# Performance work log

Measured on AMD Instinct MI355X. Metric: run time of the kernel, lower is better.

Reference implementation:

```python
import jax, jax.numpy as jnp
import numpy as np
import math

D_MODEL = 512
H = 8
D_K = D_MODEL // H


def setup_inputs() -> dict:
    key = jax.random.key(0)
    ks = jax.random.split(key, 12)
    B, T = 4, 1024
    q = jax.random.normal(ks[0], (B, T, D_MODEL), jnp.float32)
    k = jax.random.normal(ks[1], (B, T, D_MODEL), jnp.float32)
    v = jax.random.normal(ks[2], (B, T, D_MODEL), jnp.float32)
    mask = jnp.ones((B, T), jnp.int32)
    prev = jax.random.normal(ks[3], (B, H, T, T), jnp.float32)
    s = 1.0 / math.sqrt(D_MODEL)
    w_q = jax.random.normal(ks[4], (D_MODEL, D_MODEL), jnp.float32) * s
    w_k = jax.random.normal(ks[5], (D_MODEL, D_MODEL), jnp.float32) * s
    w_v = jax.random.normal(ks[6], (D_MODEL, D_MODEL), jnp.float32) * s
    w_o = jax.random.normal(ks[7], (D_MODEL, D_MODEL), jnp.float32) * s
    # Conv2d weights: torch layout OIHW; init std=0.01 per _init_conv_weights
    tw = jax.random.normal(ks[8], (H, H, 3, 3), jnp.float32) * 0.01
    tb = jnp.zeros((H,), jnp.float32)
    aw = jax.random.normal(ks[9], (H, 2 * H, 3, 3), jnp.float32) * 0.01
    ab = jnp.zeros((H,), jnp.float32)
    return {"q": q, "k": k, "v": v, "mask": mask, "previous_attention_scores": prev,
            "w_q": w_q, "w_k": w_k, "w_v": w_v, "w_o": w_o,
            "tw": tw, "tb": tb, "aw": aw, "ab": ab}


def _conv2d(x, w, b):
    # x: [B,C,T,T], w: [O,I,3,3] (torch OIHW), padding=1
    y = jax.lax.conv_general_dilated(
        x, w, window_strides=(1, 1), padding=((1, 1), (1, 1)),
        dimension_numbers=("NCHW", "OIHW", "NCHW"))
    return y + b[None, :, None, None]


def reference(q, k, v, mask, previous_attention_scores, w_q, w_k, w_v, w_o, tw, tb, aw, ab):
    B, T, _ = q.shape
    # torch Linear: y = x @ W^T  (W is [out,in])
    query = (q @ w_q.T).reshape(B, T, H, D_K).transpose(0, 2, 1, 3)  # [B,H,T,d_k]
    key = (k @ w_k.T).reshape(B, T, H, D_K).transpose(0, 2, 1, 3)
    value = (v @ w_v.T).reshape(B, T, H, D_K).transpose(0, 2, 1, 3)

    M = jnp.einsum("bhqd,bhkd->bhqk", query, key)  # [B,H,T,T]
    Mt = _conv2d(previous_attention_scores, tw, tb)
    Ma = _conv2d(jnp.concatenate((M, Mt), axis=1), aw, ab)

    A = Ma / math.sqrt(D_K)
    m = mask[:, None, None, :]  # [B,1,1,T]
    A = jnp.where(m == 0, -1e9, A)
    A = jax.nn.softmax(A, axis=-1)

    out = jnp.einsum("bhqk,bhkd->bhqd", A, value)
    out = out.transpose(0, 2, 1, 3).reshape(B, T, D_MODEL)
    return out @ w_o.T, A
```

## Files before the change

### kernel.cpp

```cpp
#include <hip/hip_runtime.h>
#include <hip/hip_bf16.h>

#define B_ 4
#define T_ 1024
#define DM 512
#define H_ 8
#define DK 64

typedef __attribute__((ext_vector_type(4))) float f32x4;
typedef __attribute__((ext_vector_type(8))) short bf16x8;

__device__ __forceinline__ unsigned short f2bf(float f) {
  __hip_bfloat16 h = __float2bfloat16(f);
  return *reinterpret_cast<unsigned short*>(&h);
}

__device__ __forceinline__ void split2(float x, short& hi, short& lo) {
  unsigned short h = f2bf(x);
  float fh = __uint_as_float(((unsigned)h) << 16);
  unsigned short l = f2bf(x - fh);
  hi = (short)h; lo = (short)l;
}

template<int OMODE, int OUTBF>
__global__ __launch_bounds__(256)
void proj_mfma(const float* __restrict__ X, const float* __restrict__ W,
               void* __restrict__ outv, int M, int N, int K) {
  float* out = (float*)outv;
  unsigned short* outb = (unsigned short*)outv;
  __shared__ __align__(16) unsigned short Ah[2048], Al[2048];
  __shared__ __align__(16) unsigned short Bh[2048], Bl[2048];
  const int t = threadIdx.x;
  const int n0 = blockIdx.x * 64, m0 = blockIdx.y * 64;
  const int wave = t >> 6, lane = t & 63;
  const int lrow = lane & 15, quad = lane >> 4;
  const int wm = wave & 1, wn = wave >> 1;
  const int srow = t >> 2, skc = t & 3;
  const int sbase = srow * 32 + ((skc ^ ((srow >> 1) & 3)) * 8);
  const int cswz = quad ^ ((lrow >> 1) & 3);
  f32x4 acc[2][2] = {};

  for (int k0 = 0; k0 < K; k0 += 32) {
    {
      const float* p = &X[(long)(m0 + srow) * K + k0 + skc * 8];
      float4 v0 = *(const float4*)p, v1 = *(const float4*)(p + 4);
      float xs[8] = {v0.x, v0.y, v0.z, v0.w, v1.x, v1.y, v1.z, v1.w};
      bf16x8 hh, ll;
#pragma unroll
      for (int i = 0; i < 8; ++i) { short h, l; split2(xs[i], h, l); hh[i] = h; ll[i] = l; }
      *(bf16x8*)&Ah[sbase] = hh; *(bf16x8*)&Al[sbase] = ll;
    }
    {
      const float* p = &W[(long)(n0 + srow) * K + k0 + skc * 8];
      float4 v0 = *(const float4*)p, v1 = *(const float4*)(p + 4);
      float xs[8] = {v0.x, v0.y, v0.z, v0.w, v1.x, v1.y, v1.z, v1.w};
      bf16x8 hh, ll;
#pragma unroll
      for (int i = 0; i < 8; ++i) { short h, l; split2(xs[i], h, l); hh[i] = h; ll[i] = l; }
      *(bf16x8*)&Bh[sbase] = hh; *(bf16x8*)&Bl[sbase] = ll;
    }
    __syncthreads();
    bf16x8 ahv[2], alv[2], bhv[2], blv[2];
#pragma unroll
    for (int f = 0; f < 2; ++f) {
      int ra = (wm * 32 + f * 16 + lrow) * 32 + cswz * 8;
      ahv[f] = *(const bf16x8*)&Ah[ra];
      alv[f] = *(const bf16x8*)&Al[ra];
      int rb = (wn * 32 + f * 16 + lrow) * 32 + cswz * 8;
      bhv[f] = *(const bf16x8*)&Bh[rb];
      blv[f] = *(const bf16x8*)&Bl[rb];
    }
#pragma unroll
    for (int fi = 0; fi < 2; ++fi)
#pragma unroll
      for (int fj = 0; fj < 2; ++fj) {
        acc[fi][fj] = __builtin_amdgcn_mfma_f32_16x16x32_bf16(alv[fi], bhv[fj], acc[fi][fj], 0, 0, 0);
        acc[fi][fj] = __builtin_amdgcn_mfma_f32_16x16x32_bf16(ahv[fi], blv[fj], acc[fi][fj], 0, 0, 0);
        acc[fi][fj] = __builtin_amdgcn_mfma_f32_16x16x32_bf16(ahv[fi], bhv[fj], acc[fi][fj], 0, 0, 0);
      }
    __syncthreads();
  }

#pragma unroll
  for (int fi = 0; fi < 2; ++fi)
#pragma unroll
    for (int fj = 0; fj < 2; ++fj)
#pragma unroll
      for (int r = 0; r < 4; ++r) {
        int row = m0 + wm * 32 + fi * 16 + quad * 4 + r;
        int col = n0 + wn * 32 + fj * 16 + lrow;
        float v = acc[fi][fj][r];
        if (OMODE == 0) {
          out[(long)row * N + col] = v;
        } else {
          int b = row >> 10, tt = row & 1023, h = col >> 6, d = col & 63;
          long off = ((long)(b * H_ + h) * T_ + tt) * DK + d;
          if (OUTBF) outb[off] = f2bf(v);
          else       out[off] = v;
        }
      }
}

__global__ __launch_bounds__(256)
void softmax_av(float* __restrict__ A, const float* __restrict__ Vp,
                float* __restrict__ ctx, const int* __restrict__ mask) {
  __shared__ __align__(16) unsigned short Ah[2048], Al[2048];
  __shared__ __align__(16) unsigned short Bh[2048], Bl[2048];
  __shared__ float sm[64][4], ss[64][4];
  const int t = threadIdx.x;
  const int bh = blockIdx.y, b = bh >> 3, h = bh & 7;
  const int m0 = blockIdx.x * 64;
  A += (long)bh * T_ * T_;
  const float* V = Vp + (long)bh * T_ * DK;
  const int wave = t >> 6, lane = t & 63;
  const int lrow = lane & 15, quad = lane >> 4;
  const int wm = wave & 1, wn = wave >> 1;
  const int srow = t >> 2, skc = t & 3;
  float* arow_p = &A[(long)(m0 + srow) * T_];

  float pm = -3.0e38f, ps = 0.f;
  {
    const int cb = skc * 256;
    for (int c = 0; c < 256; c += 4) {
      float4 v = *(const float4*)&arow_p[cb + c];
      int4 mk = *(const int4*)&mask[b * T_ + cb + c];
      float x0 = mk.x ? v.x : -1e9f;
      float x1 = mk.y ? v.y : -1e9f;
      float x2 = mk.z ? v.z : -1e9f;
      float x3 = mk.w ? v.w : -1e9f;
      float m4 = fmaxf(fmaxf(x0, x1), fmaxf(x2, x3));
      if (m4 > pm) { ps *= __expf(pm - m4); pm = m4; }
      ps += __expf(x0 - pm) + __expf(x1 - pm) + __expf(x2 - pm) + __expf(x3 - pm);
    }
  }
  sm[srow][skc] = pm; ss[srow][skc] = ps;
  __syncthreads();
  const float rmx = fmaxf(fmaxf(sm[srow][0], sm[srow][1]),
                          fmaxf(sm[srow][2], sm[srow][3]));
  const float rsum = ss[srow][0] * __expf(sm[srow][0] - rmx)
                   + ss[srow][1] * __expf(sm[srow][1] - rmx)
                   + ss[srow][2] * __expf(sm[srow][2] - rmx)
                   + ss[srow][3] * __expf(sm[srow][3] - rmx);
  const float rinv = 1.0f / rsum;

  const int sbase = srow * 32 + ((skc ^ ((srow >> 1) & 3)) * 8);
  const int vn = t & 63, vkg = t >> 6;
  const int bbase = vn * 32 + ((vkg ^ ((vn >> 1) & 3)) * 8);
  const int cswz = quad ^ ((lrow >> 1) & 3);
  f32x4 acc[2][2] = {};

  for (int k0 = 0; k0 < T_; k0 += 32) {
    __syncthreads();
    {
      float* p = &arow_p[k0 + skc * 8];
      float4 v0 = *(const float4*)p, v1 = *(const float4*)(p + 4);
      int4 mk0 = *(const int4*)&mask[b * T_ + k0 + skc * 8];
      int4 mk1 = *(const int4*)&mask[b * T_ + k0 + skc * 8 + 4];
      float e[8];
      e[0] = __expf((mk0.x ? v0.x : -1e9f) - rmx) * rinv;
      e[1] = __expf((mk0.y ? v0.y : -1e9f) - rmx) * rinv;
      e[2] = __expf((mk0.z ? v0.z : -1e9f) - rmx) * rinv;
      e[3] = __expf((mk0.w ? v0.w : -1e9f) - rmx) * rinv;
      e[4] = __expf((mk1.x ? v1.x : -1e9f) - rmx) * rinv;
      e[5] = __expf((mk1.y ? v1.y : -1e9f) - rmx) * rinv;
      e[6] = __expf((mk1.z ? v1.z : -1e9f) - rmx) * rinv;
      e[7] = __expf((mk1.w ? v1.w : -1e9f) - rmx) * rinv;
      *(float4*)p = make_float4(e[0], e[1], e[2], e[3]);
      *(float4*)(p + 4) = make_float4(e[4], e[5], e[6], e[7]);
      bf16x8 hh, ll;
#pragma unroll
      for (int i = 0; i < 8; ++i) { short hi_, lo_; split2(e[i], hi_, lo_); hh[i] = hi_; ll[i] = lo_; }
      *(bf16x8*)&Ah[sbase] = hh; *(bf16x8*)&Al[sbase] = ll;
    }
    {
      bf16x8 hh, ll;
#pragma unroll
      for (int j = 0; j < 8; ++j) {
        float x = V[(long)(k0 + vkg * 8 + j) * DK + vn];
        short hi_, lo_; split2(x, hi_, lo_); hh[j] = hi_; ll[j] = lo_;
      }
      *(bf16x8*)&Bh[bbase] = hh; *(bf16x8*)&Bl[bbase] = ll;
    }
    __syncthreads();
    bf16x8 ahv[2], alv[2], bhv[2], blv[2];
#pragma unroll
    for (int f = 0; f < 2; ++f) {
      int ra = (wm * 32 + f * 16 + lrow) * 32 + cswz * 8;
      ahv[f] = *(const bf16x8*)&Ah[ra];
      alv[f] = *(const bf16x8*)&Al[ra];
      int rb = (wn * 32 + f * 16 + lrow) * 32 + cswz * 8;
      bhv[f] = *(const bf16x8*)&Bh[rb];
      blv[f] = *(const bf16x8*)&Bl[rb];
    }
#pragma unroll
    for (int fi = 0; fi < 2; ++fi)
#pragma unroll
      for (int fj = 0; fj < 2; ++fj) {
        acc[fi][fj] = __builtin_amdgcn_mfma_f32_16x16x32_bf16(alv[fi], bhv[fj], acc[fi][fj], 0, 0, 0);
        acc[fi][fj] = __builtin_amdgcn_mfma_f32_16x16x32_bf16(ahv[fi], blv[fj], acc[fi][fj], 0, 0, 0);
        acc[fi][fj] = __builtin_amdgcn_mfma_f32_16x16x32_bf16(ahv[fi], bhv[fj], acc[fi][fj], 0, 0, 0);
      }
  }

#pragma unroll
  for (int fi = 0; fi < 2; ++fi)
#pragma unroll
    for (int fj = 0; fj < 2; ++fj)
#pragma unroll
      for (int r = 0; r < 4; ++r) {
        int row = m0 + wm * 32 + fi * 16 + quad * 4 + r;
        int col = wn * 32 + fj * 16 + lrow;
        ctx[(long)(b * T_ + row) * DM + h * DK + col] = acc[fi][fj][r];
      }
}

__global__ __launch_bounds__(512, 4)
void fused_logits(const unsigned short* __restrict__ Qp,
                  const unsigned short* __restrict__ Kp,
                  const float* __restrict__ prev,
                  const float* __restrict__ tw, const float* __restrict__ tb,
                  const float* __restrict__ aw, const float* __restrict__ ab,
                  float* __restrict__ logits) {
  __shared__ __align__(16) unsigned short SM[34816];
  unsigned short* QKl = SM;
  unsigned short* C   = SM;
  unsigned short* P   = SM + 18496;

  const int t = threadIdx.x;
  const int b = blockIdx.z, q0 = blockIdx.y * 32, k0 = blockIdx.x * 32;
  const int wave = t >> 6, lane = t & 63;
  const int lrow = lane & 15, quad = lane >> 4;
  const int o = lrow;

  bf16x8 W2f[5], W1f[3];
#pragma unroll
  for (int ks = 0; ks < 5; ++ks) {
    int kk0 = ks * 32 + quad * 8;
    bf16x8 f = {0, 0, 0, 0, 0, 0, 0, 0};
    if (o < 8 && kk0 < 144) {
      int tap = kk0 >> 4, ib = kk0 & 15;
#pragma unroll
      for (int j = 0; j < 8; ++j)
        f[j] = (short)f2bf(aw[o * 144 + (ib + j) * 9 + tap]);
    }
    W2f[ks] = f;
  }
#pragma unroll
  for (int ks = 0; ks < 3; ++ks) {
    int kk0 = ks * 32 + quad * 8;
    bf16x8 f = {0, 0, 0, 0, 0, 0, 0, 0};
    if (o < 8 && kk0 < 72) {
      int tap = kk0 >> 3;
#pragma unroll
      for (int j = 0; j < 8; ++j)
        f[j] = (short)f2bf(tw[o * 72 + j * 9 + tap]);
    }
    W1f[ks] = f;
  }
  const float tb_r = (o < 8) ? tb[o] : 0.f;
  const float ab_r = (o < 8) ? ab[o] : 0.f;

  for (int c = t; c < 4352; c += 512) {
    int seg = c & 7;
    int rc = c >> 3;
    int ha = rc / 34;
    int row = rc - ha * 34;
    int h = ha >> 1, arr = ha & 1;
    int srow = (arr ? k0 : q0) - 1 + row;
    bf16x8 v = {0, 0, 0, 0, 0, 0, 0, 0};
    if (srow >= 0 && srow < T_) {
      const unsigned short* src =
          (arr ? Kp : Qp) + ((long)((b * H_ + h) * T_ + srow)) * DK + seg * 8;
      v = *(const bf16x8*)src;
    }
    *(bf16x8*)&QKl[rc * 64 + ((seg ^ (row & 7)) * 8)] = v;
  }
  __syncthreads();

  const int hp = wave & 3;
  const int hb = hp * 4;
  unsigned mbuf[5][4];
#pragma unroll
  for (int s = 0; s < 5; ++s) {
    int tile = (wave >> 2) + 2 * s;
    if (tile <= 8) {
      int ti = tile / 3, tj = tile - ti * 3;
      int rA = ti * 16 + lrow; rA = rA > 33 ? 33 : rA;
      int rB = tj * 16 + lrow; rB = rB > 33 ? 33 : rB;
      const unsigned short* pA0 = &QKl[((hb + 0) * 34 + rA) * 64];
      const unsigned short* pB0 = &QKl[((hb + 1) * 34 + rB) * 64];
      const unsigned short* pA1 = &QKl[((hb + 2) * 34 + rA) * 64];
      const unsigned short* pB1 = &QKl[((hb + 3) * 34 + rB) * 64];
      const int swA = rA & 7, swB = rB & 7;
      f32x4 acc0 = {0.f, 0.f, 0.f, 0.f};
      f32x4 acc1 = {0.f, 0.f, 0.f, 0.f};
#pragma unroll
      for (int c = 0; c < 2; ++c) {
        int sr = c * 4 + quad;
        bf16x8 a0 = *(const bf16x8*)&pA0[(sr ^ swA) * 8];
        bf16x8 b0 = *(const bf16x8*)&pB0[(sr ^ swB) * 8];
        acc0 = __builtin_amdgcn_mfma_f32_16x16x32_bf16(a0, b0, acc0, 0, 0, 0);
        bf16x8 a1 = *(const bf16x8*)&pA1[(sr ^ swA) * 8];
        bf16x8 b1 = *(const bf16x8*)&pB1[(sr ^ swB) * 8];
        acc1 = __builtin_amdgcn_mfma_f32_16x16x32_bf16(a1, b1, acc1, 0, 0, 0);
      }
#pragma unroll
      for (int r = 0; r < 4; ++r)
        mbuf[s][r] =
            (unsigned)f2bf(acc0[r]) | ((unsigned)f2bf(acc1[r]) << 16);
    }
  }
  __syncthreads();

#pragma unroll
  for (int s = 0; s < 5; ++s) {
    int tile = (wave >> 2) + 2 * s;
    if (tile <= 8) {
      int ti = tile / 3, tj = tile - ti * 3;
#pragma unroll
      for (int r = 0; r < 4; ++r) {
        int row = ti * 16 + quad * 4 + r, col = tj * 16 + lrow;
        if (row < 34 && col < 34) {
          int pix = row * 34 + col;
          int slot = pix ^ ((pix >> 2) & 3);
          *(unsigned*)&C[slot * 16 + (pix & 1) * 8 + hp * 2] = mbuf[s][r];
        }
      }
    }
  }

  for (int u = t; u < 648; u += 512) {
    int p2 = u * 2;
    int row = p2 / 36, col = p2 - row * 36;
    int gy = q0 - 2 + row, gx = k0 - 2 + col;
    bf16x8 v0 = {0, 0, 0, 0, 0, 0, 0, 0};
    bf16x8 v1 = {0, 0, 0, 0, 0, 0, 0, 0};
    if (gy >= 0 && gy < T_) {
      const float* src = prev + ((long)(b * H_) * T_ + gy) * T_ + gx;
      bool ia = (gx >= 0 && gx < T_), ib = (gx + 1 >= 0 && gx + 1 < T_);
      if (ia && ib) {
#pragma unroll
        for (int ch = 0; ch < 8; ++ch) {
          float2 w = *(const float2*)&src[(long)ch * T_ * T_];
          v0[ch] = (short)f2bf(w.x);
          v1[ch] = (short)f2bf(w.y);
        }
      } else {
        if (ia) {
#pragma unroll
          for (int ch = 0; ch < 8; ++ch)
            v0[ch] = (short)f2bf(src[(long)ch * T_ * T_]);
        }
        if (ib) {
#pragma unroll
          for (int ch = 0; ch < 8; ++ch)
            v1[ch] = (short)f2bf(src[(long)ch * T_ * T_ + 1]);
        }
      }
    }
    *(bf16x8*)&P[p2 * 8] = v0;
    *(bf16x8*)&P[(p2 + 1) * 8] = v1;
  }
  __syncthreads();

  for (int mt = wave; mt < 73; mt += 8) {
    int pin = mt * 16 + lrow;
    if (pin > 1155) pin = 1155;
    int yi = pin / 34, xi = pin - yi * 34;
    f32x4 acc = {0.f, 0.f, 0.f, 0.f};
#pragma unroll
    for (int ks = 0; ks < 3; ++ks) {
      int tap = ks * 4 + quad;
      if (tap > 8) tap = 8;
      int dy = tap / 3, dx = tap - dy * 3;
      bf16x8 av = *(const bf16x8*)&P[((yi + dy) * 36 + xi + dx) * 8];
      acc = __builtin_amdgcn_mfma_f32_16x16x32_bf16(av, W1f[ks], acc, 0, 0, 0);
    }
#pragma unroll
    for (int r = 0; r < 4; ++r) {
      int po = mt * 16 + quad * 4 + r;
      if (o < 8 && po < 1156) {
        int yo = po / 34, xo = po - yo * 34;
        int gy = q0 - 1 + yo, gx = k0 - 1 + xo;
        float val = (gy >= 0 && gy < T_ && gx >= 0 && gx < T_) ? acc[r] + tb_r
                                                               : 0.f;
        int slot = po ^ ((po >> 2) & 3);
        C[slot * 16 + ((po & 1) ^ 1) * 8 + o] = f2bf(val);
      }
    }
  }
  __syncthreads();

  for (int mt = wave; mt < 64; mt += 8) {
    int pin = mt * 16 + lrow;
    int yi = pin >> 5, xi = pin & 31;
    f32x4 acc = {0.f, 0.f, 0.f, 0.f};
#pragma unroll
    for (int ks = 0; ks < 5; ++ks) {
      int tap = ks * 2 + (quad >> 1);
      if (tap > 8) tap = 8;
      int dy = tap / 3, dx = tap - dy * 3;
      int p2 = (yi + dy) * 34 + (xi + dx);
      int slot = p2 ^ ((p2 >> 2) & 3);
      bf16x8 av =
          *(const bf16x8*)&C[slot * 16 + (((quad & 1) ^ (p2 & 1))) * 8];
      acc = __builtin_amdgcn_mfma_f32_16x16x32_bf16(av, W2f[ks], acc, 0, 0, 0);
    }
#pragma unroll
    for (int r = 0; r < 4; ++r) {
      int po = mt * 16 + quad * 4 + r;
      if (o < 8) {
        int yo = po >> 5, xo = po & 31;
        logits[((long)(b * H_ + o) * T_ + q0 + yo) * T_ + k0 + xo] =
            (acc[r] + ab_r) * 0.125f;
      }
    }
  }
}

extern "C" void kernel_launch(void* const* d_in, const int* in_sizes, int n_in,
                              void* d_out, int out_size, void* d_ws,
                              size_t ws_size, hipStream_t stream) {
  const float* q    = (const float*)d_in[0];
  const float* k    = (const float*)d_in[1];
  const float* v    = (const float*)d_in[2];
  const int*   mask = (const int*)  d_in[3];
  const float* prev = (const float*)d_in[4];
  const float* w_q  = (const float*)d_in[5];
  const float* w_k  = (const float*)d_in[6];
  const float* w_v  = (const float*)d_in[7];
  const float* w_o  = (const float*)d_in[8];
  const float* tw   = (const float*)d_in[9];
  const float* tb   = (const float*)d_in[10];
  const float* aw   = (const float*)d_in[11];
  const float* ab   = (const float*)d_in[12];

  float* out  = (float*)d_out;
  float* Aout = out + (long)B_ * T_ * DM;

  char* wsb = (char*)d_ws;
  unsigned short* Qp = (unsigned short*)wsb;
  unsigned short* Kp = (unsigned short*)(wsb + (4L << 20));
  float* Vp  = (float*)(wsb + (8L << 20));
  float* ctx = (float*)(wsb + (16L << 20));

  dim3 blk(256);

  proj_mfma<1, 1><<<dim3(8, 64), blk, 0, stream>>>(q, w_q, Qp, 4096, 512, 512);
  proj_mfma<1, 1><<<dim3(8, 64), blk, 0, stream>>>(k, w_k, Kp, 4096, 512, 512);
  proj_mfma<1, 0><<<dim3(8, 64), blk, 0, stream>>>(v, w_v, Vp, 4096, 512, 512);

  fused_logits<<<dim3(32, 32, 4), dim3(512), 0, stream>>>(Qp, Kp, prev, tw, tb,
                                                          aw, ab, Aout);

  softmax_av<<<dim3(16, 32), blk, 0, stream>>>(Aout, Vp, ctx, mask);

  proj_mfma<0, 0><<<dim3(8, 64), blk, 0, stream>>>(ctx, w_o, out, 4096, 512, 512);
}
```

Before: 620.9 us.

## Split softmax row stats into separate kernel and prefetch prev early in logits

```diff
diff --git a/kernel.cpp b/kernel.cpp
--- a/kernel.cpp
+++ b/kernel.cpp
@@ -102,11 +102,41 @@
 }
 
 __global__ __launch_bounds__(256)
+void row_reduce(const float* __restrict__ A, const int* __restrict__ mask,
+                float2* __restrict__ stats) {
+  const int t = threadIdx.x;
+  const int wave = t >> 6, lane = t & 63;
+  const long row = (long)blockIdx.x * 4 + wave;
+  const int b = (int)(row >> 13);
+  const float* rp = A + row * T_;
+  const int* mp = mask + b * T_;
+  float x[16];
+#pragma unroll
+  for (int j = 0; j < 4; ++j) {
+    float4 v = *(const float4*)&rp[(j * 64 + lane) * 4];
+    int4 m = *(const int4*)&mp[(j * 64 + lane) * 4];
+    x[j * 4 + 0] = m.x ? v.x : -1e9f;
+    x[j * 4 + 1] = m.y ? v.y : -1e9f;
+    x[j * 4 + 2] = m.z ? v.z : -1e9f;
+    x[j * 4 + 3] = m.w ? v.w : -1e9f;
+  }
+  float mx = x[0];
+#pragma unroll
+  for (int j = 1; j < 16; ++j) mx = fmaxf(mx, x[j]);
+  for (int of = 32; of > 0; of >>= 1) mx = fmaxf(mx, __shfl_xor(mx, of, 64));
+  float s = 0.f;
+#pragma unroll
+  for (int j = 0; j < 16; ++j) s += __expf(x[j] - mx);
+  for (int of = 32; of > 0; of >>= 1) s += __shfl_xor(s, of, 64);
+  if (lane == 0) stats[row] = make_float2(mx, 1.0f / s);
+}
+
+__global__ __launch_bounds__(256)
 void softmax_av(float* __restrict__ A, const float* __restrict__ Vp,
-                float* __restrict__ ctx, const int* __restrict__ mask) {
+                float* __restrict__ ctx, const int* __restrict__ mask,
+                const float2* __restrict__ stats) {
   __shared__ __align__(16) unsigned short Ah[2048], Al[2048];
   __shared__ __align__(16) unsigned short Bh[2048], Bl[2048];
-  __shared__ float sm[64][4], ss[64][4];
   const int t = threadIdx.x;
   const int bh = blockIdx.y, b = bh >> 3, h = bh & 7;
   const int m0 = blockIdx.x * 64;
@@ -118,30 +148,8 @@
   const int srow = t >> 2, skc = t & 3;
   float* arow_p = &A[(long)(m0 + srow) * T_];
 
-  float pm = -3.0e38f, ps = 0.f;
-  {
-    const int cb = skc * 256;
-    for (int c = 0; c < 256; c += 4) {
-      float4 v = *(const float4*)&arow_p[cb + c];
-      int4 mk = *(const int4*)&mask[b * T_ + cb + c];
-      float x0 = mk.x ? v.x : -1e9f;
-      float x1 = mk.y ? v.y : -1e9f;
-      float x2 = mk.z ? v.z : -1e9f;
-      float x3 = mk.w ? v.w : -1e9f;
-      float m4 = fmaxf(fmaxf(x0, x1), fmaxf(x2, x3));
-      if (m4 > pm) { ps *= __expf(pm - m4); pm = m4; }
-      ps += __expf(x0 - pm) + __expf(x1 - pm) + __expf(x2 - pm) + __expf(x3 - pm);
-    }
-  }
-  sm[srow][skc] = pm; ss[srow][skc] = ps;
-  __syncthreads();
-  const float rmx = fmaxf(fmaxf(sm[srow][0], sm[srow][1]),
-                          fmaxf(sm[srow][2], sm[srow][3]));
-  const float rsum = ss[srow][0] * __expf(sm[srow][0] - rmx)
-                   + ss[srow][1] * __expf(sm[srow][1] - rmx)
-                   + ss[srow][2] * __expf(sm[srow][2] - rmx)
-                   + ss[srow][3] * __expf(sm[srow][3] - rmx);
-  const float rinv = 1.0f / rsum;
+  const float2 st = stats[(long)bh * T_ + m0 + srow];
+  const float rmx = st.x, rinv = st.y;
 
   const int sbase = srow * 32 + ((skc ^ ((srow >> 1) & 3)) * 8);
   const int vn = t & 63, vkg = t >> 6;
@@ -214,6 +222,38 @@
       }
 }
 
+__device__ __forceinline__ void prev_early(const float* __restrict__ prev,
+                                           int b, int q0, int k0, int u,
+                                           float* f, bool& ok0, bool& ok1) {
+  int p2 = u * 2;
+  int row = p2 / 36, col = p2 - row * 36;
+  int gy = q0 - 2 + row, gx = k0 - 2 + col;
+  ok0 = ok1 = false;
+  if (gy >= 0 && gy < T_) {
+    const float* src = prev + ((long)(b * H_) * T_ + gy) * T_ + gx;
+    bool ia = (gx >= 0 && gx < T_), ib = (gx + 1 >= 0 && gx + 1 < T_);
+    if (ia && ib) {
+#pragma unroll
+      for (int ch = 0; ch < 8; ++ch) {
+        float2 w = *(const float2*)&src[(long)ch * T_ * T_];
+        f[ch * 2] = w.x; f[ch * 2 + 1] = w.y;
+      }
+      ok0 = ok1 = true;
+    } else {
+      if (ia) {
+#pragma unroll
+        for (int ch = 0; ch < 8; ++ch) f[ch * 2] = src[(long)ch * T_ * T_];
+        ok0 = true;
+      }
+      if (ib) {
+#pragma unroll
+        for (int ch = 0; ch < 8; ++ch) f[ch * 2 + 1] = src[(long)ch * T_ * T_ + 1];
+        ok1 = true;
+      }
+    }
+  }
+}
+
 __global__ __launch_bounds__(512, 4)
 void fused_logits(const unsigned short* __restrict__ Qp,
                   const unsigned short* __restrict__ Kp,
@@ -231,6 +271,11 @@
   const int wave = t >> 6, lane = t & 63;
   const int lrow = lane & 15, quad = lane >> 4;
   const int o = lrow;
+
+  float pvA[16], pvB[16];
+  bool okA0, okA1, okB0 = false, okB1 = false;
+  prev_early(prev, b, q0, k0, t, pvA, okA0, okA1);
+  if (t < 136) prev_early(prev, b, q0, k0, t + 512, pvB, okB0, okB1);
 
   bf16x8 W2f[5], W1f[3];
 #pragma unroll
@@ -329,34 +374,32 @@
     }
   }
 
-  for (int u = t; u < 648; u += 512) {
-    int p2 = u * 2;
-    int row = p2 / 36, col = p2 - row * 36;
-    int gy = q0 - 2 + row, gx = k0 - 2 + col;
+  {
+    int p2 = t * 2;
     bf16x8 v0 = {0, 0, 0, 0, 0, 0, 0, 0};
     bf16x8 v1 = {0, 0, 0, 0, 0, 0, 0, 0};
-    if (gy >= 0 && gy < T_) {
-      const float* src = prev + ((long)(b * H_) * T_ + gy) * T_ + gx;
-      bool ia = (gx >= 0 && gx < T_), ib = (gx + 1 >= 0 && gx + 1 < T_);
-      if (ia && ib) {
-#pragma unroll
-        for (int ch = 0; ch < 8; ++ch) {
-          float2 w = *(const float2*)&src[(long)ch * T_ * T_];
-          v0[ch] = (short)f2bf(w.x);
-          v1[ch] = (short)f2bf(w.y);
-        }
-      } else {
-        if (ia) {
-#pragma unroll
-          for (int ch = 0; ch < 8; ++ch)
-            v0[ch] = (short)f2bf(src[(long)ch * T_ * T_]);
-        }
-        if (ib) {
-#pragma unroll
-          for (int ch = 0; ch < 8; ++ch)
-            v1[ch] = (short)f2bf(src[(long)ch * T_ * T_ + 1]);
-        }
-      }
+    if (okA0) {
+#pragma unroll
+      for (int ch = 0; ch < 8; ++ch) v0[ch] = (short)f2bf(pvA[ch * 2]);
+    }
+    if (okA1) {
+#pragma unroll
+      for (int ch = 0; ch < 8; ++ch) v1[ch] = (short)f2bf(pvA[ch * 2 + 1]);
+    }
+    *(bf16x8*)&P[p2 * 8] = v0;
+    *(bf16x8*)&P[(p2 + 1) * 8] = v1;
+  }
+  if (t < 136) {
+    int p2 = (t + 512) * 2;
+    bf16x8 v0 = {0, 0, 0, 0, 0, 0, 0, 0};
+    bf16x8 v1 = {0, 0, 0, 0, 0, 0, 0, 0};
+    if (okB0) {
+#pragma unroll
+      for (int ch = 0; ch < 8; ++ch) v0[ch] = (short)f2bf(pvB[ch * 2]);
+    }
+    if (okB1) {
+#pragma unroll
+      for (int ch = 0; ch < 8; ++ch) v1[ch] = (short)f2bf(pvB[ch * 2 + 1]);
     }
     *(bf16x8*)&P[p2 * 8] = v0;
     *(bf16x8*)&P[(p2 + 1) * 8] = v1;
@@ -376,17 +419,20 @@
       bf16x8 av = *(const bf16x8*)&P[((yi + dy) * 36 + xi + dx) * 8];
       acc = __builtin_amdgcn_mfma_f32_16x16x32_bf16(av, W1f[ks], acc, 0, 0, 0);
     }
+    int po0 = mt * 16 + quad * 4;
+    int yo = po0 / 34, xo = po0 - yo * 34;
 #pragma unroll
     for (int r = 0; r < 4; ++r) {
-      int po = mt * 16 + quad * 4 + r;
+      int po = po0 + r;
       if (o < 8 && po < 1156) {
-        int yo = po / 34, xo = po - yo * 34;
         int gy = q0 - 1 + yo, gx = k0 - 1 + xo;
         float val = (gy >= 0 && gy < T_ && gx >= 0 && gx < T_) ? acc[r] + tb_r
                                                                : 0.f;
         int slot = po ^ ((po >> 2) & 3);
         C[slot * 16 + ((po & 1) ^ 1) * 8 + o] = f2bf(val);
       }
+      xo++;
+      if (xo == 34) { xo = 0; yo++; }
     }
   }
   __syncthreads();
@@ -443,6 +489,7 @@
   unsigned short* Kp = (unsigned short*)(wsb + (4L << 20));
   float* Vp  = (float*)(wsb + (8L << 20));
   float* ctx = (float*)(wsb + (16L << 20));
+  float2* stats = (float2*)wsb;
 
   dim3 blk(256);
 
@@ -453,7 +500,9 @@
   fused_logits<<<dim3(32, 32, 4), dim3(512), 0, stream>>>(Qp, Kp, prev, tw, tb,
                                                           aw, ab, Aout);
 
-  softmax_av<<<dim3(16, 32), blk, 0, stream>>>(Aout, Vp, ctx, mask);
+  row_reduce<<<dim3(8192), blk, 0, stream>>>(Aout, mask, stats);
+
+  softmax_av<<<dim3(16, 32), blk, 0, stream>>>(Aout, Vp, ctx, mask, stats);
 
   proj_mfma<0, 0><<<dim3(8, 64), blk, 0, stream>>>(ctx, w_o, out, 4096, 512, 512);
 }
```

New measurement: 620.0 us. Within noise of the previous version (-0.1%).
